# Optimization experiments

Hardware: AMD Instinct MI355X
Metric: run time of the kernel (lower is better)

Reference implementation:

```python
import jax, jax.numpy as jnp
import numpy as np

N, E, D_IN, D, D_OUT, L = 50000, 800000, 128, 256, 64, 3
TAU0 = 0.5
LN_EPS = 1e-5


def setup_inputs() -> dict:
    key = jax.random.key(0)
    ks = jax.random.split(key, 16)
    u01 = jax.random.uniform(ks[2], (L, 2, N, 2), minval=1e-6, maxval=1.0 - 1e-6)
    gumbel = -jnp.log(-jnp.log(u01))  # standard Gumbel(0,1) noise, one draw per layer per action net
    s = lambda k, shape, fan: jax.random.normal(k, shape) * np.float32(1.0 / np.sqrt(fan))
    return {
        'x': jax.random.normal(ks[0], (N, D_IN), dtype=jnp.float32),
        'edge_index': jax.random.randint(ks[1], (2, E), 0, N),
        'gumbel_noise': gumbel,
        'W_enc': s(ks[3], (D_IN, D), D_IN), 'b_enc': jnp.zeros((D,), jnp.float32),
        'W_root': s(ks[4], (L, D, D), D), 'W_agg': s(ks[5], (L, D, D), D), 'b_env': jnp.zeros((L, D), jnp.float32),
        'Wa_in_r': s(ks[6], (D, 2), D), 'Wa_in_a': s(ks[7], (D, 2), D), 'b_in': jnp.zeros((2,), jnp.float32),
        'Wa_out_r': s(ks[8], (D, 2), D), 'Wa_out_a': s(ks[9], (D, 2), D), 'b_out': jnp.zeros((2,), jnp.float32),
        'Wt_r': s(ks[10], (D, 1), D), 'Wt_a': s(ks[11], (D, 1), D), 'b_t': jnp.zeros((1,), jnp.float32),
        'ln_g': jnp.ones((D,), jnp.float32), 'ln_b': jnp.zeros((D,), jnp.float32),
        'W_dec': s(ks[12], (D, D_OUT), D), 'b_dec': jnp.zeros((D_OUT,), jnp.float32),
    }


def reference(x, edge_index, gumbel_noise, W_enc, b_enc, W_root, W_agg, b_env,
              Wa_in_r, Wa_in_a, b_in, Wa_out_r, Wa_out_a, b_out,
              Wt_r, Wt_a, b_t, ln_g, ln_b, W_dec, b_dec):
    n = x.shape[0]
    u, v = edge_index[0], edge_index[1]  # message flows v -> u (aggregate at u)

    def conv(h, Wr, Wa, b, ew=None):
        # GraphConv-style: root transform + sum-aggregated (optionally edge-weighted) neighbor transform
        msg = h[v] if ew is None else ew[:, None] * h[v]  # [E, D]
        agg = jax.ops.segment_sum(msg, u, num_segments=n)  # [N, D]
        return h @ Wr + agg @ Wa + b

    def layernorm(h):
        m = jnp.mean(h, axis=-1, keepdims=True)
        var = jnp.mean((h - m) ** 2, axis=-1, keepdims=True)
        return (h - m) * jax.lax.rsqrt(var + LN_EPS) * ln_g + ln_b

    def gumbel_hard(logits, g, temp):
        # hard gumbel-softmax with straight-through estimator, per-node temperature
        y = jax.nn.softmax((logits + g) / temp, axis=-1)
        hard = jax.nn.one_hot(jnp.argmax(y, axis=-1), 2, dtype=y.dtype)
        return hard + y - jax.lax.stop_gradient(y)

    # env encoder + (dropout=identity) + relu
    h = jax.nn.relu(x @ W_enc + b_enc)

    for l in range(W_root.shape[0]):
        h = layernorm(h)
        in_logits = conv(h, Wa_in_r, Wa_in_a, b_in)    # [N, 2]
        out_logits = conv(h, Wa_out_r, Wa_out_a, b_out)  # [N, 2]
        t = conv(h, Wt_r, Wt_a, b_t)                   # [N, 1]
        temp = 1.0 / (jax.nn.softplus(t) + TAU0)       # TempSoftPlus: per-node inverse temperature
        in_prob = gumbel_hard(in_logits, gumbel_noise[l, 0], temp)
        out_prob = gumbel_hard(out_logits, gumbel_noise[l, 1], temp)
        ew = in_prob[:, 0][u] * out_prob[:, 0][v]      # [E] gated edge weights
        h = jax.nn.relu(conv(h, W_root[l], W_agg[l], b_env[l], ew))

    h = layernorm(h)
    return h @ W_dec + b_dec
```

## Files before the change

### kernel.cpp

```cpp
#include <hip/hip_runtime.h>
#include <cstdint>

#define NN 50000
#define EE 800000
#define DIN 128
#define DD 256
#define DOUT 64
#define NLAYERS 3
#define LN_EPS 1e-5f
#define NB_SCAN ((NN + 255) / 256)

typedef __attribute__((ext_vector_type(8))) _Float16 h8;
typedef __attribute__((ext_vector_type(4))) _Float16 h4;
typedef __attribute__((ext_vector_type(4))) float f4;

__device__ __forceinline__ float waveSum(float v) {
#pragma unroll
  for (int m = 1; m < 64; m <<= 1) v += __shfl_xor(v, m, 64);
  return v;
}

__device__ __forceinline__ void splith(const float4& a, const float4& b, h8& p1, h8& p2) {
  float t[8] = {a.x, a.y, a.z, a.w, b.x, b.y, b.z, b.w};
#pragma unroll
  for (int i = 0; i < 8; ++i) {
    _Float16 x = (_Float16)t[i];
    p1[i] = x;
    p2[i] = (_Float16)(t[i] - (float)x);
  }
}

__device__ __forceinline__ void split4(const float4& a, h4& q1, h4& q2) {
  float t[4] = {a.x, a.y, a.z, a.w};
#pragma unroll
  for (int i = 0; i < 4; ++i) {
    _Float16 x = (_Float16)t[i];
    q1[i] = x;
    q2[i] = (_Float16)(t[i] - (float)x);
  }
}

__global__ __launch_bounds__(256) void k_ln_scalars(
    const float* __restrict__ h, const float* __restrict__ ln_g, const float* __restrict__ ln_b,
    const float* __restrict__ Wir, const float* __restrict__ Wia,
    const float* __restrict__ Wor, const float* __restrict__ Woa,
    _Float16* __restrict__ hn1, _Float16* __restrict__ hn2,
    float* __restrict__ SR, float* __restrict__ SA) {
  const int lane = threadIdx.x & 63;
  const int node = blockIdx.x * 4 + (threadIdx.x >> 6);
  if (node >= NN) return;
  const float4 hv = *(const float4*)(h + (size_t)node * DD + lane * 4);
  float m = waveSum(hv.x + hv.y + hv.z + hv.w) * (1.f / DD);
  float dx = hv.x - m, dy = hv.y - m, dz = hv.z - m, dw = hv.w - m;
  float var = waveSum(dx * dx + dy * dy + dz * dz + dw * dw) * (1.f / DD);
  float rs = 1.f / sqrtf(var + LN_EPS);
  const float4 g = *(const float4*)(ln_g + lane * 4);
  const float4 bb = *(const float4*)(ln_b + lane * 4);
  float4 o;
  o.x = fmaf(dx * rs, g.x, bb.x);
  o.y = fmaf(dy * rs, g.y, bb.y);
  o.z = fmaf(dz * rs, g.z, bb.z);
  o.w = fmaf(dw * rs, g.w, bb.w);
  {
    h4 q1, q2;
    split4(o, q1, q2);
    *(h4*)(hn1 + (size_t)node * DD + lane * 4) = q1;
    *(h4*)(hn2 + (size_t)node * DD + lane * 4) = q2;
  }
  float p[8];
  const float4 a0 = *(const float4*)(Wir + 8 * lane);
  const float4 a1 = *(const float4*)(Wir + 8 * lane + 4);
  p[0] = o.x * a0.x + o.y * a0.z + o.z * a1.x + o.w * a1.z;
  p[1] = o.x * a0.y + o.y * a0.w + o.z * a1.y + o.w * a1.w;
  const float4 c0 = *(const float4*)(Wia + 8 * lane);
  const float4 c1 = *(const float4*)(Wia + 8 * lane + 4);
  p[2] = o.x * c0.x + o.y * c0.z + o.z * c1.x + o.w * c1.z;
  p[3] = o.x * c0.y + o.y * c0.w + o.z * c1.y + o.w * c1.w;
  const float4 e0 = *(const float4*)(Wor + 8 * lane);
  const float4 e1 = *(const float4*)(Wor + 8 * lane + 4);
  p[4] = o.x * e0.x + o.y * e0.z + o.z * e1.x + o.w * e1.z;
  p[5] = o.x * e0.y + o.y * e0.w + o.z * e1.y + o.w * e1.w;
  const float4 f0 = *(const float4*)(Woa + 8 * lane);
  const float4 f1 = *(const float4*)(Woa + 8 * lane + 4);
  p[6] = o.x * f0.x + o.y * f0.z + o.z * f1.x + o.w * f1.z;
  p[7] = o.x * f0.y + o.y * f0.w + o.z * f1.y + o.w * f1.w;
#pragma unroll
  for (int j = 0; j < 8; ++j) p[j] = waveSum(p[j]);
  if (lane == 0) {
    *(float4*)(SR + (size_t)node * 4) = make_float4(p[0], p[1], p[4], p[5]);
    *(float4*)(SA + (size_t)node * 4) = make_float4(p[2], p[3], p[6], p[7]);
  }
}

__global__ void k_zero_deg(int* __restrict__ deg) {
  int i = blockIdx.x * 256 + threadIdx.x;
  if (i < NN) deg[i] = 0;
}

__global__ void k_deg(const int* __restrict__ ei, int* __restrict__ deg) {
  int e = blockIdx.x * 256 + threadIdx.x;
  if (e < EE) atomicAdd(&deg[ei[e]], 1);
}

__global__ __launch_bounds__(256) void k_scan1(const int* __restrict__ deg,
                                               int* __restrict__ bsum) {
  __shared__ int sm[256];
  const int t = threadIdx.x;
  int i = blockIdx.x * 256 + t;
  sm[t] = (i < NN) ? deg[i] : 0;
  __syncthreads();
  for (int off = 128; off > 0; off >>= 1) {
    if (t < off) sm[t] += sm[t + off];
    __syncthreads();
  }
  if (t == 0) bsum[blockIdx.x] = sm[0];
}

__global__ __launch_bounds__(256) void k_scan2(const int* __restrict__ bsum,
                                               int* __restrict__ boff,
                                               int* __restrict__ rowptr) {
  __shared__ int sm[256];
  const int t = threadIdx.x;
  int v = (t < NB_SCAN) ? bsum[t] : 0;
  sm[t] = v;
  __syncthreads();
  for (int off = 1; off < 256; off <<= 1) {
    int x = (t >= off) ? sm[t - off] : 0;
    __syncthreads();
    sm[t] += x;
    __syncthreads();
  }
  if (t < NB_SCAN) boff[t] = sm[t] - v;
  if (t == 0) rowptr[NN] = sm[255];
}

__global__ __launch_bounds__(256) void k_scan3(const int* __restrict__ deg,
                                               const int* __restrict__ boff,
                                               int* __restrict__ rowptr,
                                               int* __restrict__ cursor) {
  __shared__ int sm[256];
  const int t = threadIdx.x;
  int i = blockIdx.x * 256 + t;
  int v = (i < NN) ? deg[i] : 0;
  sm[t] = v;
  __syncthreads();
  for (int off = 1; off < 256; off <<= 1) {
    int x = (t >= off) ? sm[t - off] : 0;
    __syncthreads();
    sm[t] += x;
    __syncthreads();
  }
  if (i < NN) {
    int r = boff[blockIdx.x] + sm[t] - v;
    rowptr[i] = r;
    cursor[i] = r;
  }
}

__global__ void k_fill(const int* __restrict__ ei, int* __restrict__ cursor,
                       int* __restrict__ csr_v) {
  int e = blockIdx.x * 256 + threadIdx.x;
  if (e >= EE) return;
  int u = ei[e], v = ei[EE + e];
  int slot = atomicAdd(&cursor[u], 1);
  csr_v[slot] = v;
}

__global__ void k_prep_conv(const float* __restrict__ Wr, const float* __restrict__ Wa,
                            _Float16* __restrict__ W1, _Float16* __restrict__ W2) {
  int idx = blockIdx.x * 256 + threadIdx.x;
  if (idx >= NLAYERS * DD * 2 * DD) return;
  int l = idx >> 17;
  int rem = idx & 131071;
  int n = rem >> 9, k = rem & 511;
  float w = (k < DD) ? Wr[((size_t)l * DD + k) * DD + n]
                     : Wa[((size_t)l * DD + (k - DD)) * DD + n];
  _Float16 x = (_Float16)w;
  W1[idx] = x;
  W2[idx] = (_Float16)(w - (float)x);
}

__global__ void k_prep_ed(const float* __restrict__ We, const float* __restrict__ Wd,
                          _Float16* __restrict__ E1, _Float16* __restrict__ E2,
                          _Float16* __restrict__ D1, _Float16* __restrict__ D2) {
  int idx = blockIdx.x * 256 + threadIdx.x;
  if (idx < DIN * DD) {
    int n = idx / DIN, k = idx - n * DIN;
    float w = We[(size_t)k * DD + n];
    _Float16 x = (_Float16)w;
    E1[idx] = x;
    E2[idx] = (_Float16)(w - (float)x);
  } else if (idx < DIN * DD + DD * DOUT) {
    int j = idx - DIN * DD;
    int n = j / DD, k = j - n * DD;
    float w = Wd[(size_t)k * DOUT + n];
    _Float16 x = (_Float16)w;
    D1[j] = x;
    D2[j] = (_Float16)(w - (float)x);
  }
}

__global__ __launch_bounds__(256) void k_gates_csr(
    const int* __restrict__ rowptr, const int* __restrict__ csr_v,
    const float* __restrict__ SR, const float* __restrict__ SA,
    const float* __restrict__ gn, const float* __restrict__ b_in,
    const float* __restrict__ b_out, unsigned char* __restrict__ gin,
    unsigned char* __restrict__ gout, int l) {
  int u = blockIdx.x * 256 + threadIdx.x;
  if (u >= NN) return;
  int beg = rowptr[u], end = rowptr[u + 1];
  float4 a = make_float4(0.f, 0.f, 0.f, 0.f);
  for (int j = beg; j < end; ++j) {
    int v = csr_v[j];
    float4 s = *(const float4*)(SA + (size_t)v * 4);
    a.x += s.x; a.y += s.y; a.z += s.z; a.w += s.w;
  }
  float4 r = *(const float4*)(SR + (size_t)u * 4);
  const float* gi = gn + ((size_t)(l * 2 + 0) * NN + u) * 2;
  const float* go = gn + ((size_t)(l * 2 + 1) * NN + u) * 2;
  float li0 = r.x + a.x + b_in[0] + gi[0];
  float li1 = r.y + a.y + b_in[1] + gi[1];
  gin[u] = (li0 >= li1) ? 1 : 0;
  float lo0 = r.z + a.z + b_out[0] + go[0];
  float lo1 = r.w + a.w + b_out[1] + go[1];
  gout[u] = (lo0 >= lo1) ? 1 : 0;
}

__global__ __launch_bounds__(256) void k_wagg_csr(
    const int* __restrict__ rowptr, const int* __restrict__ csr_v,
    const unsigned char* __restrict__ gin, const unsigned char* __restrict__ gout,
    const _Float16* __restrict__ hn1, const _Float16* __restrict__ hn2,
    _Float16* __restrict__ agg1, _Float16* __restrict__ agg2) {
  const int lane = threadIdx.x & 63;
  const int u = blockIdx.x * 4 + (threadIdx.x >> 6);
  if (u >= NN) return;
  float4 acc = make_float4(0.f, 0.f, 0.f, 0.f);
  float4 acc2 = make_float4(0.f, 0.f, 0.f, 0.f);
  if (gin[u]) {
    int beg = rowptr[u], end = rowptr[u + 1];
    for (int j0 = beg; j0 < end; j0 += 64) {
      int rem = end - j0;
      int v = -1;
      if (lane < rem) v = csr_v[j0 + lane];
      int ok = (v >= 0) ? (int)gout[v] : 0;
      unsigned long long mask = __ballot(ok);
      while (mask) {
        int l0 = __builtin_ctzll(mask);
        mask &= mask - 1;
        int vv0 = __shfl(v, l0);
        const h4* p0a = (const h4*)(hn1 + (size_t)vv0 * DD + lane * 4);
        const h4* p0b = (const h4*)(hn2 + (size_t)vv0 * DD + lane * 4);
        if (mask) {
          int l1 = __builtin_ctzll(mask);
          mask &= mask - 1;
          int vv1 = __shfl(v, l1);
          const h4* p1a = (const h4*)(hn1 + (size_t)vv1 * DD + lane * 4);
          const h4* p1b = (const h4*)(hn2 + (size_t)vv1 * DD + lane * 4);
          h4 a0 = *p0a, b0 = *p0b, a1 = *p1a, b1 = *p1b;
          acc.x += (float)a0[0] + (float)b0[0]; acc.y += (float)a0[1] + (float)b0[1];
          acc.z += (float)a0[2] + (float)b0[2]; acc.w += (float)a0[3] + (float)b0[3];
          acc2.x += (float)a1[0] + (float)b1[0]; acc2.y += (float)a1[1] + (float)b1[1];
          acc2.z += (float)a1[2] + (float)b1[2]; acc2.w += (float)a1[3] + (float)b1[3];
        } else {
          h4 a0 = *p0a, b0 = *p0b;
          acc.x += (float)a0[0] + (float)b0[0]; acc.y += (float)a0[1] + (float)b0[1];
          acc.z += (float)a0[2] + (float)b0[2]; acc.w += (float)a0[3] + (float)b0[3];
        }
      }
    }
    acc.x += acc2.x; acc.y += acc2.y; acc.z += acc2.z; acc.w += acc2.w;
  }
  h4 q1, q2;
  split4(acc, q1, q2);
  *(h4*)(agg1 + (size_t)u * DD + lane * 4) = q1;
  *(h4*)(agg2 + (size_t)u * DD + lane * 4) = q2;
}

#define BM 64
#define LDP 40

template <int KTOT, int ASTR, int NFN, int OSTR, bool RELU, bool FP16A, bool DUAL>
__global__ __launch_bounds__(256, 4) void k_mfma_gemm(
    const float* __restrict__ Af,
    const _Float16* __restrict__ A1a, const _Float16* __restrict__ A2a,
    const _Float16* __restrict__ A1b, const _Float16* __restrict__ A2b,
    const _Float16* __restrict__ B1, const _Float16* __restrict__ B2,
    const float* __restrict__ bias, float* __restrict__ outp) {
  constexpr int BN = NFN * 32;
  constexpr int KSTEPS = KTOT / 32;
  __shared__ _Float16 lA1[BM * LDP], lA2[BM * LDP];
  __shared__ _Float16 lB1[BN * LDP], lB2[BN * LDP];
  const int tid = threadIdx.x;
  const int j0 = blockIdx.x * BN;
  const int i0 = blockIdx.y * BM;
  const int lane = tid & 63, w = tid >> 6;
  const int wr = w >> 1, wc = w & 1;
  const int fr = lane & 15, fs = (lane >> 4) * 8;
  const int asr = tid >> 2, asc = (tid & 3) * 8;
  int ga = i0 + asr;
  if (ga >= NN) ga = NN - 1;
  const int bsr = (BN == 128) ? (tid >> 1) : (tid >> 2);
  const int bsc = (BN == 128) ? ((tid & 1) * 16) : ((tid & 3) * 8);
  const size_t boff = (size_t)(j0 + bsr) * KTOT + bsc;

  f4 acc[2][NFN];
#pragma unroll
  for (int i = 0; i < 2; ++i)
#pragma unroll
    for (int j = 0; j < NFN; ++j) acc[i][j] = (f4){0.f, 0.f, 0.f, 0.f};

  float4 fa0, fa1;
  h8 ra1, ra2;
  h8 rb1a, rb1b, rb2a, rb2b;
  {
    if constexpr (FP16A) {
      ra1 = *(const h8*)(A1a + (size_t)ga * ASTR + asc);
      ra2 = *(const h8*)(A2a + (size_t)ga * ASTR + asc);
    } else {
      const float* pa = Af + (size_t)ga * ASTR + asc;
      fa0 = *(const float4*)(pa);
      fa1 = *(const float4*)(pa + 4);
    }
    rb1a = *(const h8*)(B1 + boff);
    rb2a = *(const h8*)(B2 + boff);
    if constexpr (BN == 128) {
      rb1b = *(const h8*)(B1 + boff + 8);
      rb2b = *(const h8*)(B2 + boff + 8);
    }
  }
  for (int kt = 0; kt < KSTEPS; ++kt) {
    __syncthreads();
    {
      int o = asr * LDP + asc;
      if constexpr (FP16A) {
        *(h8*)&lA1[o] = ra1;
        *(h8*)&lA2[o] = ra2;
      } else {
        h8 p1, p2;
        splith(fa0, fa1, p1, p2);
        *(h8*)&lA1[o] = p1;
        *(h8*)&lA2[o] = p2;
      }
      int ob = bsr * LDP + bsc;
      *(h8*)&lB1[ob] = rb1a;
      *(h8*)&lB2[ob] = rb2a;
      if constexpr (BN == 128) {
        *(h8*)&lB1[ob + 8] = rb1b;
        *(h8*)&lB2[ob + 8] = rb2b;
      }
    }
    __syncthreads();
    if (kt < KSTEPS - 1) {
      int kb = (kt + 1) * 32;
      if constexpr (FP16A) {
        const _Float16 *s1, *s2;
        int kk;
        if constexpr (DUAL) {
          s1 = (kb < DD) ? A1a : A1b;
          s2 = (kb < DD) ? A2a : A2b;
          kk = kb & (DD - 1);
        } else {
          s1 = A1a; s2 = A2a; kk = kb;
        }
        ra1 = *(const h8*)(s1 + (size_t)ga * ASTR + kk + asc);
        ra2 = *(const h8*)(s2 + (size_t)ga * ASTR + kk + asc);
      } else {
        const float* pa = Af + (size_t)ga * ASTR + kb + asc;
        fa0 = *(const float4*)(pa);
        fa1 = *(const float4*)(pa + 4);
      }
      rb1a = *(const h8*)(B1 + boff + kb);
      rb2a = *(const h8*)(B2 + boff + kb);
      if constexpr (BN == 128) {
        rb1b = *(const h8*)(B1 + boff + kb + 8);
        rb2b = *(const h8*)(B2 + boff + kb + 8);
      }
    }
    h8 a1[2], a2[2];
#pragma unroll
    for (int mi = 0; mi < 2; ++mi) {
      int r = (wr * 32 + mi * 16 + fr) * LDP + fs;
      a1[mi] = *(const h8*)&lA1[r];
      a2[mi] = *(const h8*)&lA2[r];
    }
#pragma unroll
    for (int ni = 0; ni < NFN; ++ni) {
      int c = (wc * (NFN * 16) + ni * 16 + fr) * LDP + fs;
      h8 b1 = *(const h8*)&lB1[c];
      h8 b2 = *(const h8*)&lB2[c];
#pragma unroll
      for (int mi = 0; mi < 2; ++mi) {
        acc[mi][ni] = __builtin_amdgcn_mfma_f32_16x16x32_f16(a1[mi], b1, acc[mi][ni], 0, 0, 0);
        acc[mi][ni] = __builtin_amdgcn_mfma_f32_16x16x32_f16(a1[mi], b2, acc[mi][ni], 0, 0, 0);
        acc[mi][ni] = __builtin_amdgcn_mfma_f32_16x16x32_f16(a2[mi], b1, acc[mi][ni], 0, 0, 0);
      }
    }
  }
#pragma unroll
  for (int ni = 0; ni < NFN; ++ni) {
    int col = j0 + wc * (NFN * 16) + ni * 16 + fr;
    float bv = bias[col];
#pragma unroll
    for (int mi = 0; mi < 2; ++mi) {
      int rbase = i0 + wr * 32 + mi * 16 + (lane >> 4) * 4;
#pragma unroll
      for (int r = 0; r < 4; ++r) {
        int row = rbase + r;
        if (row < NN) {
          float v = acc[mi][ni][r] + bv;
          outp[(size_t)row * OSTR + col] = RELU ? fmaxf(v, 0.f) : v;
        }
      }
    }
  }
}

extern "C" void kernel_launch(void* const* d_in, const int* in_sizes, int n_in,
                              void* d_out, int out_size, void* d_ws, size_t ws_size,
                              hipStream_t stream) {
  const float* x = (const float*)d_in[0];
  const int* ei = (const int*)d_in[1];
  const float* gn = (const float*)d_in[2];
  const float* W_enc = (const float*)d_in[3];
  const float* b_enc = (const float*)d_in[4];
  const float* W_root = (const float*)d_in[5];
  const float* W_agg = (const float*)d_in[6];
  const float* b_env = (const float*)d_in[7];
  const float* Wa_in_r = (const float*)d_in[8];
  const float* Wa_in_a = (const float*)d_in[9];
  const float* b_in = (const float*)d_in[10];
  const float* Wa_out_r = (const float*)d_in[11];
  const float* Wa_out_a = (const float*)d_in[12];
  const float* b_out = (const float*)d_in[13];
  const float* ln_g = (const float*)d_in[17];
  const float* ln_b = (const float*)d_in[18];
  const float* W_dec = (const float*)d_in[19];
  const float* b_dec = (const float*)d_in[20];
  float* out = (float*)d_out;

  float* ws = (float*)d_ws;
  size_t off = 0;
  float* h = ws + off;    off += (size_t)NN * DD;
  _Float16* hn1 = (_Float16*)(ws + off);  off += (size_t)NN * DD / 2;
  _Float16* hn2 = (_Float16*)(ws + off);  off += (size_t)NN * DD / 2;
  _Float16* agg1 = (_Float16*)(ws + off); off += (size_t)NN * DD / 2;
  _Float16* agg2 = (_Float16*)(ws + off); off += (size_t)NN * DD / 2;
  float* SR = ws + off;   off += (size_t)NN * 4;
  float* SA = ws + off;   off += (size_t)NN * 4;
  int* rowptr = (int*)(ws + off); off += (size_t)NN + 4;
  int* csr_v = (int*)(ws + off);  off += (size_t)EE;
  unsigned char* gin = (unsigned char*)(ws + off);  off += (size_t)NN / 4;
  unsigned char* gout = (unsigned char*)(ws + off); off += (size_t)NN / 4;
  _Float16* cW1 = (_Float16*)(ws + off); off += (size_t)NLAYERS * DD * DD;
  _Float16* cW2 = (_Float16*)(ws + off); off += (size_t)NLAYERS * DD * DD;
  _Float16* eW1 = (_Float16*)(ws + off); off += (size_t)DD * DIN / 2;
  _Float16* eW2 = (_Float16*)(ws + off); off += (size_t)DD * DIN / 2;
  _Float16* dW1 = (_Float16*)(ws + off); off += (size_t)DOUT * DD / 2;
  _Float16* dW2 = (_Float16*)(ws + off); off += (size_t)DOUT * DD / 2;
  if (ws_size < off * sizeof(float)) return;
  int* deg = (int*)SR;
  int* bsum = (int*)SR + NN;
  int* boffp = (int*)SR + NN + 256;
  int* cursor = (int*)SA;

  k_zero_deg<<<(NN + 255) / 256, 256, 0, stream>>>(deg);
  k_deg<<<(EE + 255) / 256, 256, 0, stream>>>(ei, deg);
  k_scan1<<<NB_SCAN, 256, 0, stream>>>(deg, bsum);
  k_scan2<<<1, 256, 0, stream>>>(bsum, boffp, rowptr);
  k_scan3<<<NB_SCAN, 256, 0, stream>>>(deg, boffp, rowptr, cursor);
  k_fill<<<(EE + 255) / 256, 256, 0, stream>>>(ei, cursor, csr_v);

  k_prep_conv<<<(NLAYERS * DD * 2 * DD + 255) / 256, 256, 0, stream>>>(W_root, W_agg, cW1, cW2);
  k_prep_ed<<<(DIN * DD + DD * DOUT + 255) / 256, 256, 0, stream>>>(W_enc, W_dec,
                                                                    eW1, eW2, dW1, dW2);

  const int gy = (NN + BM - 1) / BM;
  k_mfma_gemm<DIN, DIN, 4, DD, true, false, false><<<dim3(2, gy), 256, 0, stream>>>(
      x, nullptr, nullptr, nullptr, nullptr, eW1, eW2, b_enc, h);

  for (int l = 0; l < NLAYERS; ++l) {
    k_ln_scalars<<<(NN + 3) / 4, 256, 0, stream>>>(h, ln_g, ln_b, Wa_in_r, Wa_in_a,
                                                   Wa_out_r, Wa_out_a, hn1, hn2, SR, SA);
    k_gates_csr<<<(NN + 255) / 256, 256, 0, stream>>>(rowptr, csr_v, SR, SA, gn,
                                                      b_in, b_out, gin, gout, l);
    k_wagg_csr<<<(NN + 3) / 4, 256, 0, stream>>>(rowptr, csr_v, gin, gout,
                                                 hn1, hn2, agg1, agg2);
    k_mfma_gemm<2 * DD, DD, 4, DD, true, true, true><<<dim3(2, gy), 256, 0, stream>>>(
        nullptr, hn1, hn2, agg1, agg2,
        cW1 + (size_t)l * DD * 2 * DD, cW2 + (size_t)l * DD * 2 * DD,
        b_env + (size_t)l * DD, h);
  }

  k_ln_scalars<<<(NN + 3) / 4, 256, 0, stream>>>(h, ln_g, ln_b, Wa_in_r, Wa_in_a,
                                                 Wa_out_r, Wa_out_a, hn1, hn2, SR, SA);
  k_mfma_gemm<DD, DD, 2, DOUT, false, true, false><<<dim3(1, gy), 256, 0, stream>>>(
      nullptr, hn1, hn2, nullptr, nullptr, dW1, dW2, b_dec, out);
}
```

Baseline: 763.6 us.

## Fuse LayerNorm and gate-scalar dots into full-row GEMM epilogue, drop LDS staging

Each GEMM block now computes a full 256-wide output row tile (64 rows), so the following LayerNorm, the fp16 hi/lo split and the four gate-logit dot products are done in the epilogue. This removes the separate k_ln_scalars kernel and the fp32 h round trip through memory. The main loop also drops LDS staging and loads A and B fragments straight from global memory. Activations are double-buffered between layers. Risks: higher register pressure from 16 accumulator fragments per wave, uncoalesced scalar fp16 stores, no LDS reuse of B across waves, and variance computed as E[x^2]-m^2.

```diff
diff --git a/kernel.cpp b/kernel.cpp
--- a/kernel.cpp
+++ b/kernel.cpp
@@ -14,9 +14,11 @@
 typedef __attribute__((ext_vector_type(4))) _Float16 h4;
 typedef __attribute__((ext_vector_type(4))) float f4;
 
-__device__ __forceinline__ float waveSum(float v) {
-#pragma unroll
-  for (int m = 1; m < 64; m <<= 1) v += __shfl_xor(v, m, 64);
+__device__ __forceinline__ float red16(float v) {
+  v += __shfl_xor(v, 1, 64);
+  v += __shfl_xor(v, 2, 64);
+  v += __shfl_xor(v, 4, 64);
+  v += __shfl_xor(v, 8, 64);
   return v;
 }
 
@@ -27,68 +29,6 @@
     _Float16 x = (_Float16)t[i];
     p1[i] = x;
     p2[i] = (_Float16)(t[i] - (float)x);
-  }
-}
-
-__device__ __forceinline__ void split4(const float4& a, h4& q1, h4& q2) {
-  float t[4] = {a.x, a.y, a.z, a.w};
-#pragma unroll
-  for (int i = 0; i < 4; ++i) {
-    _Float16 x = (_Float16)t[i];
-    q1[i] = x;
-    q2[i] = (_Float16)(t[i] - (float)x);
-  }
-}
-
-__global__ __launch_bounds__(256) void k_ln_scalars(
-    const float* __restrict__ h, const float* __restrict__ ln_g, const float* __restrict__ ln_b,
-    const float* __restrict__ Wir, const float* __restrict__ Wia,
-    const float* __restrict__ Wor, const float* __restrict__ Woa,
-    _Float16* __restrict__ hn1, _Float16* __restrict__ hn2,
-    float* __restrict__ SR, float* __restrict__ SA) {
-  const int lane = threadIdx.x & 63;
-  const int node = blockIdx.x * 4 + (threadIdx.x >> 6);
-  if (node >= NN) return;
-  const float4 hv = *(const float4*)(h + (size_t)node * DD + lane * 4);
-  float m = waveSum(hv.x + hv.y + hv.z + hv.w) * (1.f / DD);
-  float dx = hv.x - m, dy = hv.y - m, dz = hv.z - m, dw = hv.w - m;
-  float var = waveSum(dx * dx + dy * dy + dz * dz + dw * dw) * (1.f / DD);
-  float rs = 1.f / sqrtf(var + LN_EPS);
-  const float4 g = *(const float4*)(ln_g + lane * 4);
-  const float4 bb = *(const float4*)(ln_b + lane * 4);
-  float4 o;
-  o.x = fmaf(dx * rs, g.x, bb.x);
-  o.y = fmaf(dy * rs, g.y, bb.y);
-  o.z = fmaf(dz * rs, g.z, bb.z);
-  o.w = fmaf(dw * rs, g.w, bb.w);
-  {
-    h4 q1, q2;
-    split4(o, q1, q2);
-    *(h4*)(hn1 + (size_t)node * DD + lane * 4) = q1;
-    *(h4*)(hn2 + (size_t)node * DD + lane * 4) = q2;
-  }
-  float p[8];
-  const float4 a0 = *(const float4*)(Wir + 8 * lane);
-  const float4 a1 = *(const float4*)(Wir + 8 * lane + 4);
-  p[0] = o.x * a0.x + o.y * a0.z + o.z * a1.x + o.w * a1.z;
-  p[1] = o.x * a0.y + o.y * a0.w + o.z * a1.y + o.w * a1.w;
-  const float4 c0 = *(const float4*)(Wia + 8 * lane);
-  const float4 c1 = *(const float4*)(Wia + 8 * lane + 4);
-  p[2] = o.x * c0.x + o.y * c0.z + o.z * c1.x + o.w * c1.z;
-  p[3] = o.x * c0.y + o.y * c0.w + o.z * c1.y + o.w * c1.w;
-  const float4 e0 = *(const float4*)(Wor + 8 * lane);
-  const float4 e1 = *(const float4*)(Wor + 8 * lane + 4);
-  p[4] = o.x * e0.x + o.y * e0.z + o.z * e1.x + o.w * e1.z;
-  p[5] = o.x * e0.y + o.y * e0.w + o.z * e1.y + o.w * e1.w;
-  const float4 f0 = *(const float4*)(Woa + 8 * lane);
-  const float4 f1 = *(const float4*)(Woa + 8 * lane + 4);
-  p[6] = o.x * f0.x + o.y * f0.z + o.z * f1.x + o.w * f1.z;
-  p[7] = o.x * f0.y + o.y * f0.w + o.z * f1.y + o.w * f1.w;
-#pragma unroll
-  for (int j = 0; j < 8; ++j) p[j] = waveSum(p[j]);
-  if (lane == 0) {
-    *(float4*)(SR + (size_t)node * 4) = make_float4(p[0], p[1], p[4], p[5]);
-    *(float4*)(SA + (size_t)node * 4) = make_float4(p[2], p[3], p[6], p[7]);
   }
 }
 
@@ -270,124 +210,94 @@
     }
     acc.x += acc2.x; acc.y += acc2.y; acc.z += acc2.z; acc.w += acc2.w;
   }
-  h4 q1, q2;
-  split4(acc, q1, q2);
-  *(h4*)(agg1 + (size_t)u * DD + lane * 4) = q1;
-  *(h4*)(agg2 + (size_t)u * DD + lane * 4) = q2;
-}
-
-#define BM 64
-#define LDP 40
-
-template <int KTOT, int ASTR, int NFN, int OSTR, bool RELU, bool FP16A, bool DUAL>
-__global__ __launch_bounds__(256, 4) void k_mfma_gemm(
+  {
+    float t[4] = {acc.x, acc.y, acc.z, acc.w};
+    h4 q1, q2;
+#pragma unroll
+    for (int i = 0; i < 4; ++i) {
+      _Float16 x = (_Float16)t[i];
+      q1[i] = x;
+      q2[i] = (_Float16)(t[i] - (float)x);
+    }
+    *(h4*)(agg1 + (size_t)u * DD + lane * 4) = q1;
+    *(h4*)(agg2 + (size_t)u * DD + lane * 4) = q2;
+  }
+}
+
+template <int KTOT, int NFN, bool FUSE_LN, bool AFP32, bool DUAL, bool RELU>
+__global__ __launch_bounds__(256) void k_gemm(
     const float* __restrict__ Af,
     const _Float16* __restrict__ A1a, const _Float16* __restrict__ A2a,
     const _Float16* __restrict__ A1b, const _Float16* __restrict__ A2b,
     const _Float16* __restrict__ B1, const _Float16* __restrict__ B2,
-    const float* __restrict__ bias, float* __restrict__ outp) {
-  constexpr int BN = NFN * 32;
-  constexpr int KSTEPS = KTOT / 32;
-  __shared__ _Float16 lA1[BM * LDP], lA2[BM * LDP];
-  __shared__ _Float16 lB1[BN * LDP], lB2[BN * LDP];
+    const float* __restrict__ bias,
+    const float* __restrict__ lng, const float* __restrict__ lnb,
+    const float* __restrict__ Wir, const float* __restrict__ Wia,
+    const float* __restrict__ Wor, const float* __restrict__ Woa,
+    _Float16* __restrict__ O1, _Float16* __restrict__ O2,
+    float* __restrict__ SR, float* __restrict__ SA,
+    float* __restrict__ Of, int ostr) {
+  constexpr int AS = AFP32 ? KTOT : DD;
   const int tid = threadIdx.x;
-  const int j0 = blockIdx.x * BN;
-  const int i0 = blockIdx.y * BM;
   const int lane = tid & 63, w = tid >> 6;
   const int wr = w >> 1, wc = w & 1;
-  const int fr = lane & 15, fs = (lane >> 4) * 8;
-  const int asr = tid >> 2, asc = (tid & 3) * 8;
-  int ga = i0 + asr;
-  if (ga >= NN) ga = NN - 1;
-  const int bsr = (BN == 128) ? (tid >> 1) : (tid >> 2);
-  const int bsc = (BN == 128) ? ((tid & 1) * 16) : ((tid & 3) * 8);
-  const size_t boff = (size_t)(j0 + bsr) * KTOT + bsc;
+  const int fr = lane & 15, g4 = lane >> 4;
+  const int fs = g4 * 8;
+  const int i0 = blockIdx.x * 64;
+
+  size_t aoff[2];
+#pragma unroll
+  for (int mi = 0; mi < 2; ++mi) {
+    int r = i0 + wr * 32 + mi * 16 + fr;
+    if (r >= NN) r = NN - 1;
+    aoff[mi] = (size_t)r * AS;
+  }
+  size_t boff[NFN];
+#pragma unroll
+  for (int ni = 0; ni < NFN; ++ni)
+    boff[ni] = (size_t)(wc * (NFN * 16) + ni * 16 + fr) * KTOT;
 
   f4 acc[2][NFN];
 #pragma unroll
-  for (int i = 0; i < 2; ++i)
-#pragma unroll
-    for (int j = 0; j < NFN; ++j) acc[i][j] = (f4){0.f, 0.f, 0.f, 0.f};
-
-  float4 fa0, fa1;
-  h8 ra1, ra2;
-  h8 rb1a, rb1b, rb2a, rb2b;
-  {
-    if constexpr (FP16A) {
-      ra1 = *(const h8*)(A1a + (size_t)ga * ASTR + asc);
-      ra2 = *(const h8*)(A2a + (size_t)ga * ASTR + asc);
+  for (int mi = 0; mi < 2; ++mi)
+#pragma unroll
+    for (int ni = 0; ni < NFN; ++ni) acc[mi][ni] = (f4){0.f, 0.f, 0.f, 0.f};
+
+#pragma unroll 4
+  for (int kt = 0; kt < KTOT / 32; ++kt) {
+    const int kb = kt * 32;
+    const int kl = kb + fs;
+    h8 a1[2], a2[2];
+    if constexpr (AFP32) {
+#pragma unroll
+      for (int mi = 0; mi < 2; ++mi) {
+        const float* pa = Af + aoff[mi] + kl;
+        float4 u = *(const float4*)(pa);
+        float4 v = *(const float4*)(pa + 4);
+        splith(u, v, a1[mi], a2[mi]);
+      }
     } else {
-      const float* pa = Af + (size_t)ga * ASTR + asc;
-      fa0 = *(const float4*)(pa);
-      fa1 = *(const float4*)(pa + 4);
+      const _Float16* p1;
+      const _Float16* p2;
+      int ko;
+      if constexpr (DUAL) {
+        bool lo = kb < DD;
+        p1 = lo ? A1a : A1b;
+        p2 = lo ? A2a : A2b;
+        ko = lo ? kl : kl - DD;
+      } else {
+        p1 = A1a; p2 = A2a; ko = kl;
+      }
+#pragma unroll
+      for (int mi = 0; mi < 2; ++mi) {
+        a1[mi] = *(const h8*)(p1 + aoff[mi] + ko);
+        a2[mi] = *(const h8*)(p2 + aoff[mi] + ko);
+      }
     }
-    rb1a = *(const h8*)(B1 + boff);
-    rb2a = *(const h8*)(B2 + boff);
-    if constexpr (BN == 128) {
-      rb1b = *(const h8*)(B1 + boff + 8);
-      rb2b = *(const h8*)(B2 + boff + 8);
-    }
-  }
-  for (int kt = 0; kt < KSTEPS; ++kt) {
-    __syncthreads();
-    {
-      int o = asr * LDP + asc;
-      if constexpr (FP16A) {
-        *(h8*)&lA1[o] = ra1;
-        *(h8*)&lA2[o] = ra2;
-      } else {
-        h8 p1, p2;
-        splith(fa0, fa1, p1, p2);
-        *(h8*)&lA1[o] = p1;
-        *(h8*)&lA2[o] = p2;
-      }
-      int ob = bsr * LDP + bsc;
-      *(h8*)&lB1[ob] = rb1a;
-      *(h8*)&lB2[ob] = rb2a;
-      if constexpr (BN == 128) {
-        *(h8*)&lB1[ob + 8] = rb1b;
-        *(h8*)&lB2[ob + 8] = rb2b;
-      }
-    }
-    __syncthreads();
-    if (kt < KSTEPS - 1) {
-      int kb = (kt + 1) * 32;
-      if constexpr (FP16A) {
-        const _Float16 *s1, *s2;
-        int kk;
-        if constexpr (DUAL) {
-          s1 = (kb < DD) ? A1a : A1b;
-          s2 = (kb < DD) ? A2a : A2b;
-          kk = kb & (DD - 1);
-        } else {
-          s1 = A1a; s2 = A2a; kk = kb;
-        }
-        ra1 = *(const h8*)(s1 + (size_t)ga * ASTR + kk + asc);
-        ra2 = *(const h8*)(s2 + (size_t)ga * ASTR + kk + asc);
-      } else {
-        const float* pa = Af + (size_t)ga * ASTR + kb + asc;
-        fa0 = *(const float4*)(pa);
-        fa1 = *(const float4*)(pa + 4);
-      }
-      rb1a = *(const h8*)(B1 + boff + kb);
-      rb2a = *(const h8*)(B2 + boff + kb);
-      if constexpr (BN == 128) {
-        rb1b = *(const h8*)(B1 + boff + kb + 8);
-        rb2b = *(const h8*)(B2 + boff + kb + 8);
-      }
-    }
-    h8 a1[2], a2[2];
-#pragma unroll
-    for (int mi = 0; mi < 2; ++mi) {
-      int r = (wr * 32 + mi * 16 + fr) * LDP + fs;
-      a1[mi] = *(const h8*)&lA1[r];
-      a2[mi] = *(const h8*)&lA2[r];
-    }
 #pragma unroll
     for (int ni = 0; ni < NFN; ++ni) {
-      int c = (wc * (NFN * 16) + ni * 16 + fr) * LDP + fs;
-      h8 b1 = *(const h8*)&lB1[c];
-      h8 b2 = *(const h8*)&lB2[c];
+      h8 b1 = *(const h8*)(B1 + boff[ni] + kl);
+      h8 b2 = *(const h8*)(B2 + boff[ni] + kl);
 #pragma unroll
       for (int mi = 0; mi < 2; ++mi) {
         acc[mi][ni] = __builtin_amdgcn_mfma_f32_16x16x32_f16(a1[mi], b1, acc[mi][ni], 0, 0, 0);
@@ -396,22 +306,138 @@
       }
     }
   }
-#pragma unroll
-  for (int ni = 0; ni < NFN; ++ni) {
-    int col = j0 + wc * (NFN * 16) + ni * 16 + fr;
-    float bv = bias[col];
+
+  if constexpr (FUSE_LN) {
+    __shared__ float rsum[64][2], rsq[64][2];
+    __shared__ float rdots[64][2][8];
+#pragma unroll
+    for (int mi = 0; mi < 2; ++mi)
+#pragma unroll
+      for (int ni = 0; ni < NFN; ++ni) {
+        int col = wc * 128 + ni * 16 + fr;
+        float bv = bias[col];
+#pragma unroll
+        for (int r = 0; r < 4; ++r) {
+          float v = acc[mi][ni][r] + bv;
+          if constexpr (RELU) v = fmaxf(v, 0.f);
+          acc[mi][ni][r] = v;
+        }
+      }
+#pragma unroll
+    for (int mi = 0; mi < 2; ++mi)
+#pragma unroll
+      for (int r = 0; r < 4; ++r) {
+        float s = 0.f, q = 0.f;
+#pragma unroll
+        for (int ni = 0; ni < NFN; ++ni) {
+          float v = acc[mi][ni][r];
+          s += v;
+          q += v * v;
+        }
+        s = red16(s);
+        q = red16(q);
+        if (fr == 0) {
+          int rl = wr * 32 + mi * 16 + g4 * 4 + r;
+          rsum[rl][wc] = s;
+          rsq[rl][wc] = q;
+        }
+      }
+    __syncthreads();
+    float mv[2][4], rv[2][4];
+#pragma unroll
+    for (int mi = 0; mi < 2; ++mi)
+#pragma unroll
+      for (int r = 0; r < 4; ++r) {
+        int rl = wr * 32 + mi * 16 + g4 * 4 + r;
+        float S = rsum[rl][0] + rsum[rl][1];
+        float Q = rsq[rl][0] + rsq[rl][1];
+        float m = S * (1.f / DD);
+        float var = fmaxf(Q * (1.f / DD) - m * m, 0.f);
+        mv[mi][r] = m;
+        rv[mi][r] = 1.f / sqrtf(var + LN_EPS);
+      }
+#pragma unroll
+    for (int mi = 0; mi < 2; ++mi)
+#pragma unroll
+      for (int ni = 0; ni < NFN; ++ni) {
+        int col = wc * 128 + ni * 16 + fr;
+        float g = lng[col], b = lnb[col];
+#pragma unroll
+        for (int r = 0; r < 4; ++r) {
+          float o = (acc[mi][ni][r] - mv[mi][r]) * rv[mi][r] * g + b;
+          acc[mi][ni][r] = o;
+          int row = i0 + wr * 32 + mi * 16 + g4 * 4 + r;
+          if (row < NN) {
+            _Float16 x = (_Float16)o;
+            O1[(size_t)row * DD + col] = x;
+            O2[(size_t)row * DD + col] = (_Float16)(o - (float)x);
+          }
+        }
+      }
 #pragma unroll
     for (int mi = 0; mi < 2; ++mi) {
-      int rbase = i0 + wr * 32 + mi * 16 + (lane >> 4) * 4;
-#pragma unroll
-      for (int r = 0; r < 4; ++r) {
-        int row = rbase + r;
-        if (row < NN) {
-          float v = acc[mi][ni][r] + bv;
-          outp[(size_t)row * OSTR + col] = RELU ? fmaxf(v, 0.f) : v;
+      float pd[4][8];
+#pragma unroll
+      for (int r = 0; r < 4; ++r)
+#pragma unroll
+        for (int j = 0; j < 8; ++j) pd[r][j] = 0.f;
+#pragma unroll
+      for (int ni = 0; ni < NFN; ++ni) {
+        int col = wc * 128 + ni * 16 + fr;
+        float2 wir = *(const float2*)(Wir + col * 2);
+        float2 wia = *(const float2*)(Wia + col * 2);
+        float2 wor = *(const float2*)(Wor + col * 2);
+        float2 woa = *(const float2*)(Woa + col * 2);
+#pragma unroll
+        for (int r = 0; r < 4; ++r) {
+          float o = acc[mi][ni][r];
+          pd[r][0] = fmaf(o, wir.x, pd[r][0]);
+          pd[r][1] = fmaf(o, wir.y, pd[r][1]);
+          pd[r][2] = fmaf(o, wia.x, pd[r][2]);
+          pd[r][3] = fmaf(o, wia.y, pd[r][3]);
+          pd[r][4] = fmaf(o, wor.x, pd[r][4]);
+          pd[r][5] = fmaf(o, wor.y, pd[r][5]);
+          pd[r][6] = fmaf(o, woa.x, pd[r][6]);
+          pd[r][7] = fmaf(o, woa.y, pd[r][7]);
+        }
+      }
+#pragma unroll
+      for (int r = 0; r < 4; ++r)
+#pragma unroll
+        for (int j = 0; j < 8; ++j) pd[r][j] = red16(pd[r][j]);
+      if (fr == 0) {
+#pragma unroll
+        for (int r = 0; r < 4; ++r) {
+          int rl = wr * 32 + mi * 16 + g4 * 4 + r;
+#pragma unroll
+          for (int j = 0; j < 8; ++j) rdots[rl][wc][j] = pd[r][j];
         }
       }
     }
+    __syncthreads();
+    if (tid < 64) {
+      int row = i0 + tid;
+      if (row < NN) {
+        float d[8];
+#pragma unroll
+        for (int j = 0; j < 8; ++j) d[j] = rdots[tid][0][j] + rdots[tid][1][j];
+        *(float4*)(SR + (size_t)row * 4) = make_float4(d[0], d[1], d[4], d[5]);
+        *(float4*)(SA + (size_t)row * 4) = make_float4(d[2], d[3], d[6], d[7]);
+      }
+    }
+  } else {
+#pragma unroll
+    for (int mi = 0; mi < 2; ++mi)
+#pragma unroll
+      for (int ni = 0; ni < NFN; ++ni) {
+        int col = wc * (NFN * 16) + ni * 16 + fr;
+        float bv = bias[col];
+#pragma unroll
+        for (int r = 0; r < 4; ++r) {
+          int row = i0 + wr * 32 + mi * 16 + g4 * 4 + r;
+          if (row < NN) Of[(size_t)row * ostr + col] = acc[mi][ni][r] + bv;
+        }
+      }
   }
 }
 
@@ -440,13 +466,14 @@
 
   float* ws = (float*)d_ws;
   size_t off = 0;
-  float* h = ws + off;    off += (size_t)NN * DD;
-  _Float16* hn1 = (_Float16*)(ws + off);  off += (size_t)NN * DD / 2;
-  _Float16* hn2 = (_Float16*)(ws + off);  off += (size_t)NN * DD / 2;
+  _Float16* hnA1 = (_Float16*)(ws + off); off += (size_t)NN * DD / 2;
+  _Float16* hnA2 = (_Float16*)(ws + off); off += (size_t)NN * DD / 2;
+  _Float16* hnB1 = (_Float16*)(ws + off); off += (size_t)NN * DD / 2;
+  _Float16* hnB2 = (_Float16*)(ws + off); off += (size_t)NN * DD / 2;
   _Float16* agg1 = (_Float16*)(ws + off); off += (size_t)NN * DD / 2;
   _Float16* agg2 = (_Float16*)(ws + off); off += (size_t)NN * DD / 2;
-  float* SR = ws + off;   off += (size_t)NN * 4;
-  float* SA = ws + off;   off += (size_t)NN * 4;
+  float* SR = ws + off; off += (size_t)NN * 4;
+  float* SA = ws + off; off += (size_t)NN * 4;
   int* rowptr = (int*)(ws + off); off += (size_t)NN + 4;
   int* csr_v = (int*)(ws + off);  off += (size_t)EE;
   unsigned char* gin = (unsigned char*)(ws + off);  off += (size_t)NN / 4;
@@ -474,25 +501,30 @@
   k_prep_ed<<<(DIN * DD + DD * DOUT + 255) / 256, 256, 0, stream>>>(W_enc, W_dec,
                                                                     eW1, eW2, dW1, dW2);
 
-  const int gy = (NN + BM - 1) / BM;
-  k_mfma_gemm<DIN, DIN, 4, DD, true, false, false><<<dim3(2, gy), 256, 0, stream>>>(
-      x, nullptr, nullptr, nullptr, nullptr, eW1, eW2, b_enc, h);
-
+  const int gb = (NN + 63) / 64;
+  k_gemm<DIN, 8, true, true, false, true><<<gb, 256, 0, stream>>>(
+      x, nullptr, nullptr, nullptr, nullptr, eW1, eW2, b_enc,
+      ln_g, ln_b, Wa_in_r, Wa_in_a, Wa_out_r, Wa_out_a,
+      hnA1, hnA2, SR, SA, nullptr, 0);
+
+  _Float16 *cur1 = hnA1, *cur2 = hnA2, *nxt1 = hnB1, *nxt2 = hnB2;
   for (int l = 0; l < NLAYERS; ++l) {
-    k_ln_scalars<<<(NN + 3) / 4, 256, 0, stream>>>(h, ln_g, ln_b, Wa_in_r, Wa_in_a,
-                                                   Wa_out_r, Wa_out_a, hn1, hn2, SR, SA);
     k_gates_csr<<<(NN + 255) / 256, 256, 0, stream>>>(rowptr, csr_v, SR, SA, gn,
                                                       b_in, b_out, gin, gout, l);
     k_wagg_csr<<<(NN + 3) / 4, 256, 0, stream>>>(rowptr, csr_v, gin, gout,
-                                                 hn1, hn2, agg1, agg2);
-    k_mfma_gemm<2 * DD, DD, 4, DD, true, true, true><<<dim3(2, gy), 256, 0, stream>>>(
-        nullptr, hn1, hn2, agg1, agg2,
+                                                 cur1, cur2, agg1, agg2);
+    k_gemm<2 * DD, 8, true, false, true, true><<<gb, 256, 0, stream>>>(
+        nullptr, cur1, cur2, agg1, agg2,
         cW1 + (size_t)l * DD * 2 * DD, cW2 + (size_t)l * DD * 2 * DD,
-        b_env + (size_t)l * DD, h);
-  }
-
-  k_ln_scalars<<<(NN + 3) / 4, 256, 0, stream>>>(h, ln_g, ln_b, Wa_in_r, Wa_in_a,
-                                                 Wa_out_r, Wa_out_a, hn1, hn2, SR, SA);
-  k_mfma_gemm<DD, DD, 2, DOUT, false, true, false><<<dim3(1, gy), 256, 0, stream>>>(
-      nullptr, hn1, hn2, nullptr, nullptr, dW1, dW2, b_dec, out);
-}
+        b_env + (size_t)l * DD,
+        ln_g, ln_b, Wa_in_r, Wa_in_a, Wa_out_r, Wa_out_a,
+        nxt1, nxt2, SR, SA, nullptr, 0);
+    _Float16* t1 = cur1; cur1 = nxt1; nxt1 = t1;
+    _Float16* t2 = cur2; cur2 = nxt2; nxt2 = t2;
+  }
+
+  k_gemm<DD, 2, false, false, false, false><<<gb, 256, 0, stream>>>(
+      nullptr, cur1, cur2, nullptr, nullptr, dW1, dW2, b_dec,
+      nullptr, nullptr, nullptr, nullptr, nullptr, nullptr,
+      nullptr, nullptr, nullptr, nullptr, out, DOUT);
+}
```

Result: slower. 1.144 ms (+49.8%).
